# Kernel optimization log

Hardware: AMD Instinct MI355X
Metric: run time of the kernel (lower is better)

The kernel has to match this reference:

```python
import jax, jax.numpy as jnp
import numpy as np

RADIUS = 0.1
K_NEIGHBOURS = 32


def setup_inputs() -> dict:
    key = jax.random.key(0)
    k1, k2, k3 = jax.random.split(key, 3)
    B, N, M, C = 4, 8192, 2048, 128
    xyz = jax.random.uniform(k1, (B, 3, N), dtype=jnp.float32)
    new_xyz = jax.random.uniform(k2, (B, 3, M), dtype=jnp.float32)
    feature = jax.random.normal(k3, (B, C, N), dtype=jnp.float32)
    return {"new_xyz": new_xyz, "xyz": xyz, "feature": feature, "use_xyz": 1}


def _ball_query(xyz, new_xyz, radius, k):
    # xyz: [B,3,N], new_xyz: [B,3,M] -> idx [B,M,k] (first-k-in-ball, padded
    # with first valid index, pointnet2 semantics), counts [B,M]
    n = xyz.shape[-1]
    # squared pairwise distance [B,M,N]
    d2 = jnp.sum((new_xyz[:, :, :, None] - xyz[:, :, None, :]) ** 2, axis=1)
    in_ball = d2 < radius * radius
    cand = jnp.where(in_ball, jnp.arange(n, dtype=jnp.int32), n)
    # smallest indices first == first-k points inside the ball
    idx_sorted = jnp.sort(cand, axis=-1)[..., :k]
    valid = idx_sorted < n
    first = idx_sorted[..., :1]
    pad = jnp.where(first < n, first, 0)  # empty ball -> index 0
    idx = jnp.where(valid, idx_sorted, pad).astype(jnp.int32)
    count = jnp.sum(valid, axis=-1).astype(jnp.int32)
    return idx, count


def _group_points(f, idx):
    # f: [B,C,N], idx: [B,M,K] -> [B,C,M,K]
    return jax.vmap(lambda fb, ib: fb[:, ib])(f, idx)


def reference(new_xyz, xyz, feature, use_xyz):
    idx, _count = _ball_query(xyz, new_xyz, RADIUS, K_NEIGHBOURS)
    group_xyz = _group_points(xyz, idx) - new_xyz[..., None]  # [B,3,M,K]
    group_feature = _group_points(feature, idx)               # [B,C,M,K]
    if use_xyz:
        group_feature = jnp.concatenate([group_xyz, group_feature], axis=1)
    return group_feature, group_xyz
```

## Files before the change

kernel.cpp:

```cpp
#include <hip/hip_runtime.h>
#include <hip/hip_bf16.h>


#define K_NEIGH 32
#define R2_F32 0.009999999776482582f
#define CCH 128
#define NPTS 8192
#define MQ 2048

__global__ __launch_bounds__(512, 8) void ball_q4_kernel(
    const float* __restrict__ xyz,
    const float* __restrict__ new_xyz,
    int* __restrict__ idxb,
    float* __restrict__ out0,
    float* __restrict__ out1,
    int use_xyz)
{
    constexpr int CH = 2048;
    __shared__ float4 pts[CH];
    __shared__ int lidx[8][4][K_NEIGH];

    const int tid  = threadIdx.x;
    const int wave = tid >> 6;
    const int lane = tid & 63;
    const int q0 = blockIdx.x * 32 + wave * 4;
    const int b  = q0 / MQ;
    const int m0 = q0 - b * MQ;

    const float* x0 = xyz + (size_t)b * 3 * NPTS;
    const float* x1 = x0 + NPTS;
    const float* x2 = x1 + NPTS;
    const float* nb = new_xyz + (size_t)b * 3 * MQ;

    float qx[4], qy[4], qz[4];
    int   cnt[4] = {0, 0, 0, 0};
    int   ff [4] = {0, 0, 0, 0};
    #pragma unroll
    for (int j = 0; j < 4; ++j) {
        qx[j] = nb[m0 + j];
        qy[j] = nb[MQ + m0 + j];
        qz[j] = nb[2 * MQ + m0 + j];
    }
    const unsigned long long below = (1ull << lane) - 1ull;

    for (int c0 = 0; c0 < NPTS; c0 += CH) {
        {
            const int p0 = tid * 4;
            const float4 vx = *(const float4*)&x0[c0 + p0];
            const float4 vy = *(const float4*)&x1[c0 + p0];
            const float4 vz = *(const float4*)&x2[c0 + p0];
            pts[p0 + 0] = make_float4(vx.x, vy.x, vz.x, 0.f);
            pts[p0 + 1] = make_float4(vx.y, vy.y, vz.y, 0.f);
            pts[p0 + 2] = make_float4(vx.z, vy.z, vz.z, 0.f);
            pts[p0 + 3] = make_float4(vx.w, vy.w, vz.w, 0.f);
        }
        __syncthreads();

        const bool alldone = (cnt[0] >= K_NEIGH) && (cnt[1] >= K_NEIGH) &&
                             (cnt[2] >= K_NEIGH) && (cnt[3] >= K_NEIGH);
        if (!alldone) {
            for (int g = 0; g < CH; g += 128) {
                const float4 pa = pts[g + lane];
                const float4 pb = pts[g + 64 + lane];
                const int gia = c0 + g + lane;

                #pragma unroll
                for (int j = 0; j < 4; ++j) {
                    #define D2(P) \
                        __fadd_rn(__fadd_rn(__fmul_rn((P).x - qx[j], (P).x - qx[j]), \
                                            __fmul_rn((P).y - qy[j], (P).y - qy[j])), \
                                  __fmul_rn((P).z - qz[j], (P).z - qz[j]))
                    const bool ina = D2(pa) < R2_F32;
                    const bool inb = D2(pb) < R2_F32;
                    #undef D2
                    const unsigned long long ma = __ballot(ina);
                    const unsigned long long mb = __ballot(inb);
                    if (ma) {
                        if (cnt[j] == 0) ff[j] = gia - lane + (__ffsll(ma) - 1);
                        if (ina) {
                            const int pos = cnt[j] + __popcll(ma & below);
                            if (pos < K_NEIGH) lidx[wave][j][pos] = gia;
                        }
                        cnt[j] += __popcll(ma);
                    }
                    if (mb) {
                        if (cnt[j] == 0) ff[j] = gia - lane + 64 + (__ffsll(mb) - 1);
                        if (inb) {
                            const int pos = cnt[j] + __popcll(mb & below);
                            if (pos < K_NEIGH) lidx[wave][j][pos] = gia + 64;
                        }
                        cnt[j] += __popcll(mb);
                    }
                }
            }
        }
        __syncthreads();
    }

    asm volatile("s_waitcnt lgkmcnt(0)" ::: "memory");

    const size_t MK = (size_t)MQ * K_NEIGH;
    #pragma unroll
    for (int j = 0; j < 4; ++j) {
        if (lane < K_NEIGH) {
            const int m = m0 + j;
            const int jdx = (lane < cnt[j]) ? lidx[wave][j][lane] : ff[j];
            idxb[((size_t)b * MQ + m) * K_NEIGH + lane] = jdx;
            const float gx = x0[jdx] - qx[j];
            const float gy = x1[jdx] - qy[j];
            const float gz = x2[jdx] - qz[j];
            const size_t o1 = (size_t)b * 3 * MK + (size_t)m * K_NEIGH + lane;
            out1[o1]          = gx;
            out1[o1 + MK]     = gy;
            out1[o1 + 2 * MK] = gz;
            if (use_xyz) {
                const size_t o0 = (size_t)b * (CCH + 3) * MK + (size_t)m * K_NEIGH + lane;
                out0[o0]          = gx;
                out0[o0 + MK]     = gy;
                out0[o0 + 2 * MK] = gz;
            }
        }
    }
}

__global__ __launch_bounds__(256) void ball_query_xyz_kernel(
    const float* __restrict__ xyz, const float* __restrict__ new_xyz,
    int* __restrict__ idxb, float* __restrict__ out0, float* __restrict__ out1,
    int N, int M, int C, int use_xyz)
{
    __shared__ int lidx[4][K_NEIGH];
    const int wave = threadIdx.x >> 6;
    const int lane = threadIdx.x & 63;
    const int q = blockIdx.x * 4 + wave;
    const int b = q / M;
    const int m = q - b * M;

    const float* xb = xyz + (size_t)b * 3 * N;
    const float* x0 = xb;
    const float* x1 = xb + N;
    const float* x2 = xb + 2 * N;
    const float* nb = new_xyz + (size_t)b * 3 * M;
    const float qx = nb[m];
    const float qy = nb[M + m];
    const float qz = nb[2 * M + m];

    int cnt = 0;
    int ff  = 0;
    const unsigned long long below = (1ull << lane) - 1ull;

    for (int t0 = 0; t0 < N; t0 += 64) {
        const int i = t0 + lane;
        const float dx = x0[i] - qx;
        const float dy = x1[i] - qy;
        const float dz = x2[i] - qz;
        const float d2 = __fadd_rn(__fadd_rn(__fmul_rn(dx, dx), __fmul_rn(dy, dy)),
                                   __fmul_rn(dz, dz));
        const bool in_ball = d2 < R2_F32;
        const unsigned long long mask = __ballot(in_ball);
        if (mask) {
            if (cnt == 0) ff = t0 + (__ffsll(mask) - 1);
            if (in_ball) {
                const int pos = cnt + __popcll(mask & below);
                if (pos < K_NEIGH) lidx[wave][pos] = i;
            }
            cnt += __popcll(mask);
            if (cnt >= K_NEIGH) break;
        }
    }

    asm volatile("s_waitcnt lgkmcnt(0)" ::: "memory");

    if (lane < K_NEIGH) {
        const int j = (lane < cnt) ? lidx[wave][lane] : ff;
        idxb[(size_t)q * K_NEIGH + lane] = j;
        const float gx = x0[j] - qx;
        const float gy = x1[j] - qy;
        const float gz = x2[j] - qz;
        const size_t MK = (size_t)M * K_NEIGH;
        const size_t o1 = (size_t)b * 3 * MK + (size_t)m * K_NEIGH + lane;
        out1[o1]          = gx;
        out1[o1 + MK]     = gy;
        out1[o1 + 2 * MK] = gz;
        if (use_xyz) {
            const size_t o0 = (size_t)b * (C + 3) * MK + (size_t)m * K_NEIGH + lane;
            out0[o0]          = gx;
            out0[o0 + MK]     = gy;
            out0[o0 + 2 * MK] = gz;
        }
    }
}

__global__ __launch_bounds__(1024, 4) void gather_onepass_kernel(
    const float* __restrict__ feat,
    const int* __restrict__ idxb,
    float* __restrict__ out0,
    int use_xyz)
{
    __shared__ float sf[2 * NPTS];

    const int t   = threadIdx.x;
    const int bid = blockIdx.x;
    const int b   = (bid & 7) >> 1;
    const int cg  = ((bid >> 3) << 1) | (bid & 1);
    const int c0  = cg * 2;

    const int4* ip4 = (const int4*)(idxb + (size_t)b * MQ * K_NEIGH);
    int4 jj[16];
    #pragma unroll
    for (int i = 0; i < 16; ++i) jj[i] = ip4[i * 1024 + t];

    const float4* fv = (const float4*)(feat + ((size_t)b * CCH + c0) * NPTS);
    #pragma unroll
    for (int r = 0; r < 4; ++r)
        ((float4*)sf)[t + r * 1024] = fv[t + r * 1024];
    __syncthreads();

    const size_t MK = (size_t)MQ * K_NEIGH;
    const int CO   = use_xyz ? (CCH + 3) : CCH;
    const int coff = use_xyz ? 3 : 0;
    float* o0 = out0 + ((size_t)b * CO + coff + c0) * MK;
    float* o1 = o0 + MK;

    #pragma unroll
    for (int i = 0; i < 16; ++i) {
        const int p = i * 4096 + 4 * t;
        const int4 j4 = jj[i];
        float4 s0, s1;
        s0.x = sf[j4.x]; s0.y = sf[j4.y]; s0.z = sf[j4.z]; s0.w = sf[j4.w];
        s1.x = sf[NPTS + j4.x]; s1.y = sf[NPTS + j4.y];
        s1.z = sf[NPTS + j4.z]; s1.w = sf[NPTS + j4.w];
        *(float4*)(o0 + p) = s0;
        *(float4*)(o1 + p) = s1;
    }
}

__global__ __launch_bounds__(256) void gather_kernel(
    const float* __restrict__ xyz, const float* __restrict__ new_xyz,
    const float* __restrict__ feat, const int* __restrict__ idxb,
    float* __restrict__ out0, float* __restrict__ out1,
    int N, int M, int C, int use_xyz)
{
    const int tid = threadIdx.x;
    const int k = tid & 31;
    const int mloc = tid >> 5;
    const int mchunks = M >> 3;
    const int b = blockIdx.x / mchunks;
    const int m = (blockIdx.x - b * mchunks) * 8 + mloc;
    const int q = b * M + m;
    const int j = idxb[(size_t)q * K_NEIGH + k];
    const size_t xb = (size_t)b * 3 * N;
    const size_t nb = (size_t)b * 3 * M;
    const float gx = xyz[xb + j]         - new_xyz[nb + m];
    const float gy = xyz[xb + N + j]     - new_xyz[nb + M + m];
    const float gz = xyz[xb + 2 * N + j] - new_xyz[nb + 2 * M + m];
    const size_t MK = (size_t)M * K_NEIGH;
    const size_t o1 = (size_t)b * 3 * MK + (size_t)m * K_NEIGH + k;
    out1[o1] = gx; out1[o1 + MK] = gy; out1[o1 + 2 * MK] = gz;
    const int CO = use_xyz ? (C + 3) : C;
    size_t o0 = (size_t)b * CO * MK + (size_t)m * K_NEIGH + k;
    if (use_xyz) {
        out0[o0] = gx; out0[o0 + MK] = gy; out0[o0 + 2 * MK] = gz;
        o0 += 3 * MK;
    }
    const float* fb = feat + (size_t)b * C * N;
    #pragma unroll 4
    for (int c = 0; c < C; c += 4) {
        const float v0 = fb[(size_t)c * N + j];
        const float v1 = fb[(size_t)(c + 1) * N + j];
        const float v2 = fb[(size_t)(c + 2) * N + j];
        const float v3 = fb[(size_t)(c + 3) * N + j];
        out0[o0 + (size_t)c * MK]       = v0;
        out0[o0 + (size_t)(c + 1) * MK] = v1;
        out0[o0 + (size_t)(c + 2) * MK] = v2;
        out0[o0 + (size_t)(c + 3) * MK] = v3;
    }
}

extern "C" void kernel_launch(void* const* d_in, const int* in_sizes, int n_in,
                              void* d_out, int out_size, void* d_ws, size_t ws_size,
                              hipStream_t stream) {
    const float* new_xyz = (const float*)d_in[0];
    const float* xyz     = (const float*)d_in[1];
    const float* feat    = (const float*)d_in[2];

    const int B = 4;
    const int M = in_sizes[0] / (3 * B);
    const int N = in_sizes[1] / (3 * B);
    const int C = in_sizes[2] / (B * N);

    const long long sz_with = (long long)B * (C + 6) * M * K_NEIGH;
    const int use_xyz = (out_size == sz_with) ? 1 : 0;

    float* out0 = (float*)d_out;
    float* out1 = out0 + (size_t)B * (use_xyz ? (C + 3) : C) * M * K_NEIGH;

    int* idxb = (int*)d_ws;
    const size_t idx_bytes = (size_t)B * M * K_NEIGH * sizeof(int);

    const bool fast = (B == 4) && (N == NPTS) && (M == MQ) && (C == CCH)
                      && (ws_size >= idx_bytes);

    if (fast) {
        ball_q4_kernel<<<(B * MQ) / 32, 512, 0, stream>>>(
            xyz, new_xyz, idxb, out0, out1, use_xyz);
        gather_onepass_kernel<<<256, 1024, 0, stream>>>(feat, idxb, out0, use_xyz);
    } else {
        ball_query_xyz_kernel<<<(B * M) / 4, 256, 0, stream>>>(
            xyz, new_xyz, idxb, out0, out1, N, M, C, use_xyz);
        gather_kernel<<<B * (M / 8), 256, 0, stream>>>(xyz, new_xyz, feat, idxb,
                                                       out0, out1, N, M, C, use_xyz);
    }
}
```

Baseline: 64.23 us.

## Split ball-query point scan across four waves per query group and merge

The ball-query kernel changes from one wave scanning all points for four queries to four waves each scanning a quarter of the points for the same four queries. Per-range counts, first-hit indices and neighbour lists go to shared memory and are merged in point order, which keeps the first-k semantics. This gives four times as many waves to hide latency. It drops the shared-memory staging of transposed point chunks in favour of direct global (cache-served) loads, and it loses the per-chunk early exit.

After: 53.46 us. 16.8% less time.

```diff
diff --git a/kernel.cpp b/kernel.cpp
--- a/kernel.cpp
+++ b/kernel.cpp
@@ -8,7 +8,7 @@
 #define NPTS 8192
 #define MQ 2048
 
-__global__ __launch_bounds__(512, 8) void ball_q4_kernel(
+__global__ __launch_bounds__(256, 8) void ball_split4_kernel(
     const float* __restrict__ xyz,
     const float* __restrict__ new_xyz,
     int* __restrict__ idxb,
@@ -16,14 +16,14 @@
     float* __restrict__ out1,
     int use_xyz)
 {
-    constexpr int CH = 2048;
-    __shared__ float4 pts[CH];
-    __shared__ int lidx[8][4][K_NEIGH];
+    __shared__ int scnt[4][4];
+    __shared__ int sff [4][4];
+    __shared__ int slidx[4][4][K_NEIGH];
 
     const int tid  = threadIdx.x;
-    const int wave = tid >> 6;
+    const int w    = tid >> 6;
     const int lane = tid & 63;
-    const int q0 = blockIdx.x * 32 + wave * 4;
+    const int q0 = blockIdx.x * 4;
     const int b  = q0 / MQ;
     const int m0 = q0 - b * MQ;
 
@@ -33,92 +33,78 @@
     const float* nb = new_xyz + (size_t)b * 3 * MQ;
 
     float qx[4], qy[4], qz[4];
-    int   cnt[4] = {0, 0, 0, 0};
-    int   ff [4] = {0, 0, 0, 0};
     #pragma unroll
     for (int j = 0; j < 4; ++j) {
         qx[j] = nb[m0 + j];
         qy[j] = nb[MQ + m0 + j];
         qz[j] = nb[2 * MQ + m0 + j];
     }
+    int cnt[4] = {0, 0, 0, 0};
+    int ff [4] = {0, 0, 0, 0};
     const unsigned long long below = (1ull << lane) - 1ull;
 
-    for (int c0 = 0; c0 < NPTS; c0 += CH) {
-        {
-            const int p0 = tid * 4;
-            const float4 vx = *(const float4*)&x0[c0 + p0];
-            const float4 vy = *(const float4*)&x1[c0 + p0];
-            const float4 vz = *(const float4*)&x2[c0 + p0];
-            pts[p0 + 0] = make_float4(vx.x, vy.x, vz.x, 0.f);
-            pts[p0 + 1] = make_float4(vx.y, vy.y, vz.y, 0.f);
-            pts[p0 + 2] = make_float4(vx.z, vy.z, vz.z, 0.f);
-            pts[p0 + 3] = make_float4(vx.w, vy.w, vz.w, 0.f);
-        }
-        __syncthreads();
-
-        const bool alldone = (cnt[0] >= K_NEIGH) && (cnt[1] >= K_NEIGH) &&
-                             (cnt[2] >= K_NEIGH) && (cnt[3] >= K_NEIGH);
-        if (!alldone) {
-            for (int g = 0; g < CH; g += 128) {
-                const float4 pa = pts[g + lane];
-                const float4 pb = pts[g + 64 + lane];
-                const int gia = c0 + g + lane;
-
-                #pragma unroll
-                for (int j = 0; j < 4; ++j) {
-                    #define D2(P) \
-                        __fadd_rn(__fadd_rn(__fmul_rn((P).x - qx[j], (P).x - qx[j]), \
-                                            __fmul_rn((P).y - qy[j], (P).y - qy[j])), \
-                                  __fmul_rn((P).z - qz[j], (P).z - qz[j]))
-                    const bool ina = D2(pa) < R2_F32;
-                    const bool inb = D2(pb) < R2_F32;
-                    #undef D2
-                    const unsigned long long ma = __ballot(ina);
-                    const unsigned long long mb = __ballot(inb);
-                    if (ma) {
-                        if (cnt[j] == 0) ff[j] = gia - lane + (__ffsll(ma) - 1);
-                        if (ina) {
-                            const int pos = cnt[j] + __popcll(ma & below);
-                            if (pos < K_NEIGH) lidx[wave][j][pos] = gia;
-                        }
-                        cnt[j] += __popcll(ma);
-                    }
-                    if (mb) {
-                        if (cnt[j] == 0) ff[j] = gia - lane + 64 + (__ffsll(mb) - 1);
-                        if (inb) {
-                            const int pos = cnt[j] + __popcll(mb & below);
-                            if (pos < K_NEIGH) lidx[wave][j][pos] = gia + 64;
-                        }
-                        cnt[j] += __popcll(mb);
-                    }
+    const int rbase = w * 2048;
+    for (int g = 0; g < 2048; g += 64) {
+        const int i = rbase + g + lane;
+        const float ax = x0[i];
+        const float ay = x1[i];
+        const float az = x2[i];
+        #pragma unroll
+        for (int j = 0; j < 4; ++j) {
+            const float d2 = __fadd_rn(__fadd_rn(__fmul_rn(ax - qx[j], ax - qx[j]),
+                                                 __fmul_rn(ay - qy[j], ay - qy[j])),
+                                       __fmul_rn(az - qz[j], az - qz[j]));
+            const bool in = d2 < R2_F32;
+            const unsigned long long mk = __ballot(in);
+            if (mk) {
+                if (cnt[j] == 0) ff[j] = rbase + g + (__ffsll(mk) - 1);
+                if (in) {
+                    const int pos = cnt[j] + __popcll(mk & below);
+                    if (pos < K_NEIGH) slidx[w][j][pos] = i;
                 }
+                cnt[j] += __popcll(mk);
             }
         }
-        __syncthreads();
-    }
-
-    asm volatile("s_waitcnt lgkmcnt(0)" ::: "memory");
-
-    const size_t MK = (size_t)MQ * K_NEIGH;
-    #pragma unroll
-    for (int j = 0; j < 4; ++j) {
-        if (lane < K_NEIGH) {
-            const int m = m0 + j;
-            const int jdx = (lane < cnt[j]) ? lidx[wave][j][lane] : ff[j];
-            idxb[((size_t)b * MQ + m) * K_NEIGH + lane] = jdx;
-            const float gx = x0[jdx] - qx[j];
-            const float gy = x1[jdx] - qy[j];
-            const float gz = x2[jdx] - qz[j];
-            const size_t o1 = (size_t)b * 3 * MK + (size_t)m * K_NEIGH + lane;
-            out1[o1]          = gx;
-            out1[o1 + MK]     = gy;
-            out1[o1 + 2 * MK] = gz;
-            if (use_xyz) {
-                const size_t o0 = (size_t)b * (CCH + 3) * MK + (size_t)m * K_NEIGH + lane;
-                out0[o0]          = gx;
-                out0[o0 + MK]     = gy;
-                out0[o0 + 2 * MK] = gz;
-            }
+    }
+
+    if (lane < 4) {
+        scnt[w][lane] = cnt[lane];
+        sff [w][lane] = ff[lane];
+    }
+    __syncthreads();
+
+    const int jq = w;
+    const float qxx = nb[m0 + jq];
+    const float qyy = nb[MQ + m0 + jq];
+    const float qzz = nb[2 * MQ + m0 + jq];
+
+    if (lane < K_NEIGH) {
+        int bacc = 0, jdx = -1, ffq = 0;
+        bool ffset = false;
+        #pragma unroll
+        for (int r = 0; r < 4; ++r) {
+            const int cr = scnt[r][jq];
+            if (!ffset && cr > 0) { ffq = sff[r][jq]; ffset = true; }
+            if (jdx < 0 && lane < bacc + cr) jdx = slidx[r][jq][lane - bacc];
+            bacc += cr;
+        }
+        if (jdx < 0) jdx = ffq;
+
+        const int m = m0 + jq;
+        idxb[((size_t)b * MQ + m) * K_NEIGH + lane] = jdx;
+        const float gx = x0[jdx] - qxx;
+        const float gy = x1[jdx] - qyy;
+        const float gz = x2[jdx] - qzz;
+        const size_t MK = (size_t)MQ * K_NEIGH;
+        const size_t o1 = (size_t)b * 3 * MK + (size_t)m * K_NEIGH + lane;
+        out1[o1]          = gx;
+        out1[o1 + MK]     = gy;
+        out1[o1 + 2 * MK] = gz;
+        if (use_xyz) {
+            const size_t o0 = (size_t)b * (CCH + 3) * MK + (size_t)m * K_NEIGH + lane;
+            out0[o0]          = gx;
+            out0[o0 + MK]     = gy;
+            out0[o0 + 2 * MK] = gz;
         }
     }
 }
@@ -301,7 +287,7 @@
                       && (ws_size >= idx_bytes);
 
     if (fast) {
-        ball_q4_kernel<<<(B * MQ) / 32, 512, 0, stream>>>(
+        ball_split4_kernel<<<(B * MQ) / 4, 256, 0, stream>>>(
             xyz, new_xyz, idxb, out0, out1, use_xyz);
         gather_onepass_kernel<<<256, 1024, 0, stream>>>(feat, idxb, out0, use_xyz);
     } else {
```
